# Performance work log

Hardware: AMD Instinct MI355X
Metric: run time of the kernel (lower is better)

## Reference

```python
import math
import jax, jax.numpy as jnp
import numpy as np

CT = {"SDD": 1000.0, "SCD": 500.0, "det_interval": 1.0, "num_det": 736}


def ramp_filter_np(ct, scale):
    # Standard equiangular fan-beam ramp filter (utility.ramp_filter):
    #   h[0] = 1/(8*db^2); h[n odd] = -1/(2*(pi*sin(n*db))^2); h[n even!=0] = 0
    db = ct["det_interval"] / ct["SDD"] * scale  # angular detector pitch at this scale
    n_det = int(ct["num_det"] // scale)
    n = np.arange(-(n_det - 1), n_det)  # length K = 2*n_det - 1
    h = np.zeros(n.shape, dtype=np.float32)
    h[n == 0] = 1.0 / (8.0 * db ** 2)
    odd = (n % 2) != 0
    h[odd] = -0.5 / (np.pi * np.sin(n[odd] * db)) ** 2
    return h


def setup_inputs() -> dict:
    key = jax.random.key(0)
    scale = 1
    batch, ch, view, det = 16, 1, 1152, CT["num_det"] // scale
    sinogram = jax.random.normal(key, (batch, ch, view, det), dtype=jnp.float32)
    delta_b = CT["det_interval"] / CT["SDD"]
    # recon_filter = ramp_filter * scale * delta_b, shaped [1,1,1,K] (OIHW)
    filt = ramp_filter_np(CT, scale) * scale * delta_b
    recon_filter = jnp.asarray(filt, dtype=jnp.float32)[None, None, None, :]
    return {"sinogram": sinogram, "recon_filter": recon_filter, "scale": scale}


def reference(sinogram, recon_filter, scale):
    det = sinogram.shape[-1]
    # cosine fan-beam pre-weighting
    s_range = (CT["det_interval"]
               * jnp.linspace((1.0 - det) / 2.0, (det - 1.0) / 2.0, det, dtype=jnp.float32)
               * scale) / CT["SDD"]
    cos_weight = (CT["SCD"] / 10000.0) * jnp.cos(s_range)  # [det]
    x = sinogram * cos_weight[None, None, None, :]
    # 1D ramp-filter convolution along detector axis (F.conv2d with 1xK kernel)
    K = recon_filter.shape[-1]
    pad = K // 2
    out = jax.lax.conv_general_dilated(
        x, recon_filter,
        window_strides=(1, 1),
        padding=[(0, 0), (pad, pad)],
        dimension_numbers=("NCHW", "OIHW", "NCHW"),
    )
    return out
```

## Files before the change

### kernel.cpp

```cpp
#include <hip/hip_runtime.h>

typedef unsigned short ushort_t;
typedef ushort_t u16x8 __attribute__((ext_vector_type(8)));
typedef __bf16 bf16x8 __attribute__((ext_vector_type(8)));
typedef float f32x4 __attribute__((ext_vector_type(4)));

#define DET 736
#define NPAD 768
#define NT 23
#define NRB 1152
#define CPB (NT * 64)


__global__ void prep_af(const float* __restrict__ sino, ushort_t* __restrict__ Af) {
    int c = blockIdx.x * blockDim.x + threadIdx.x;
    int rblk = c / CPB;
    int rem  = c - rblk * CPB;
    int t    = rem >> 6;
    int lane = rem & 63;
    int rr = lane & 15, quad = lane >> 4;
    const float* g = sino + (size_t)(rblk * 16 + rr) * DET + t * 32 + quad * 8;
    f32x4 lo = *(const f32x4*)g;
    f32x4 hi = *(const f32x4*)(g + 4);
    u16x8 v;
#pragma unroll
    for (int e = 0; e < 4; ++e) {
        v[e]     = __builtin_bit_cast(ushort_t, (__bf16)lo[e]);
        v[e + 4] = __builtin_bit_cast(ushort_t, (__bf16)hi[e]);
    }
    *(u16x8*)(Af + (size_t)c * 8) = v;
}

__global__ void prep_bf(const float* __restrict__ filt, ushort_t* __restrict__ Bf) {
    int c = blockIdx.x * blockDim.x + threadIdx.x;
    int cb  = c / CPB;
    int rem = c - cb * CPB;
    int t    = rem >> 6;
    int lane = rem & 63;
    int cc = lane & 15, quad = lane >> 4;
    int n = cb * 16 + cc;
    u16x8 v;
#pragma unroll
    for (int e = 0; e < 8; ++e) {
        int k = t * 32 + quad * 8 + e;
        float w = 0.05f * cosf(((float)k - 367.5f) * 0.001f);
        float val = (n < DET) ? filt[k - n + (DET - 1)] * w : 0.0f;
        v[e] = __builtin_bit_cast(ushort_t, (__bf16)val);
    }
    *(u16x8*)(Bf + (size_t)c * 8) = v;
}

__global__ __launch_bounds__(1024, 4) void gemm_frag(
    const ushort_t* __restrict__ Af,
    const ushort_t* __restrict__ Bf,
    float* __restrict__ C)
{
    __shared__ ushort_t Bs[4 * CPB * 8];

    const int tid  = threadIdx.x;
    const int lane = tid & 63;
    const int wid  = tid >> 6;
    const int quad = lane >> 4;
    const int l16  = lane & 15;

    const ushort_t* bsrc = Bf + (size_t)blockIdx.y * (4 * CPB * 8);
    for (int c = tid; c < 4 * CPB; c += 1024)
        *(u16x8*)(Bs + c * 8) = *(const u16x8*)(bsrc + (size_t)c * 8);
    __syncthreads();

    const int rblk0 = blockIdx.x * 64 + wid * 4;

    f32x4 acc[4][4];
#pragma unroll
    for (int i = 0; i < 4; ++i)
#pragma unroll
        for (int j = 0; j < 4; ++j)
            acc[i][j] = (f32x4){0.f, 0.f, 0.f, 0.f};

    const ushort_t* pA[4];
#pragma unroll
    for (int mi = 0; mi < 4; ++mi)
        pA[mi] = Af + ((size_t)(rblk0 + mi) * CPB + lane) * 8;
    const ushort_t* pB[4];
#pragma unroll
    for (int ni = 0; ni < 4; ++ni)
        pB[ni] = Bs + (ni * CPB + lane) * 8;

    for (int t = 0; t < NT; ++t) {
        u16x8 a[4], b[4];
#pragma unroll
        for (int mi = 0; mi < 4; ++mi)
            a[mi] = *(const u16x8*)(pA[mi] + t * 512);
#pragma unroll
        for (int ni = 0; ni < 4; ++ni)
            b[ni] = *(const u16x8*)(pB[ni] + t * 512);
#pragma unroll
        for (int mi = 0; mi < 4; ++mi)
#pragma unroll
            for (int ni = 0; ni < 4; ++ni)
                acc[mi][ni] = __builtin_amdgcn_mfma_f32_16x16x32_bf16(
                    __builtin_bit_cast(bf16x8, a[mi]),
                    __builtin_bit_cast(bf16x8, b[ni]),
                    acc[mi][ni], 0, 0, 0);
    }

    const int col0 = blockIdx.y * 64;
#pragma unroll
    for (int mi = 0; mi < 4; ++mi) {
#pragma unroll
        for (int ni = 0; ni < 4; ++ni) {
            int colg = col0 + ni * 16 + l16;
            if (colg < DET) {
#pragma unroll
                for (int r = 0; r < 4; ++r) {
                    size_t rowg = (size_t)(rblk0 + mi) * 16 + quad * 4 + r;
                    C[rowg * DET + colg] = acc[mi][ni][r];
                }
            }
        }
    }
}

extern "C" void kernel_launch(void* const* d_in, const int* in_sizes, int n_in,
                              void* d_out, int out_size, void* d_ws, size_t ws_size,
                              hipStream_t stream) {
    const float* sino = (const float*)d_in[0];
    const float* filt = (const float*)d_in[1];
    int total = in_sizes[0];
    int M = total / DET;

    ushort_t* Af = (ushort_t*)d_ws;
    ushort_t* Bf = Af + (size_t)NRB * CPB * 8;
    float* out = (float*)d_out;

    prep_af<<<(NRB * CPB) / 256, 256, 0, stream>>>(sino, Af);
    prep_bf<<<(48 * CPB) / 256, 256, 0, stream>>>(filt, Bf);

    dim3 grid(M / 1024, NPAD / 64);
    gemm_frag<<<grid, 1024, 0, stream>>>(Af, Bf, out);
}
```

Before: 138.6 us.

## Exploit ramp filter's zero even taps to split convolution into half-size parity GEMMs

The ramp filter is zero at every even nonzero offset, so each output only depends on inputs of opposite parity plus the center tap. The detector axis is split into even and odd halves, producing two half-K, half-N GEMMs (about a quarter of the MACs each), and the center tap is added in the epilogue from the original fp32 sinogram. The A fragments for the next k-step are also loaded ahead of time as a register prefetch. The cost is an extra sinogram read in the epilogue, strided stores to interleaved columns, and a more complex prep kernel.

After: 158.8 us. 1.15x slower.

```diff
diff --git a/kernel.cpp b/kernel.cpp
--- a/kernel.cpp
+++ b/kernel.cpp
@@ -6,69 +6,99 @@
 typedef float f32x4 __attribute__((ext_vector_type(4)));
 
 #define DET 736
-#define NPAD 768
-#define NT 23
+#define HALF 368
+#define HK 384
+#define NTT 12
+#define CPB2 (NTT * 64)
 #define NRB 1152
-#define CPB (NT * 64)
 
 
-__global__ void prep_af(const float* __restrict__ sino, ushort_t* __restrict__ Af) {
+__global__ void prep_af(const float* __restrict__ sino,
+                        ushort_t* __restrict__ Ae, ushort_t* __restrict__ Ao) {
     int c = blockIdx.x * blockDim.x + threadIdx.x;
-    int rblk = c / CPB;
-    int rem  = c - rblk * CPB;
-    int t    = rem >> 6;
-    int lane = rem & 63;
+    int rblk = c / CPB2;
+    int rem  = c - rblk * CPB2;
+    int t = rem >> 6, lane = rem & 63;
     int rr = lane & 15, quad = lane >> 4;
-    const float* g = sino + (size_t)(rblk * 16 + rr) * DET + t * 32 + quad * 8;
-    f32x4 lo = *(const f32x4*)g;
-    f32x4 hi = *(const f32x4*)(g + 4);
-    u16x8 v;
+    int j0 = t * 32 + quad * 8;
+    u16x8 ve, vo;
+    if (j0 < HALF) {
+        const float* g = sino + (size_t)(rblk * 16 + rr) * DET + 2 * j0;
+        float w[16];
+        *(f32x4*)(w)      = *(const f32x4*)(g);
+        *(f32x4*)(w + 4)  = *(const f32x4*)(g + 4);
+        *(f32x4*)(w + 8)  = *(const f32x4*)(g + 8);
+        *(f32x4*)(w + 12) = *(const f32x4*)(g + 12);
 #pragma unroll
-    for (int e = 0; e < 4; ++e) {
-        v[e]     = __builtin_bit_cast(ushort_t, (__bf16)lo[e]);
-        v[e + 4] = __builtin_bit_cast(ushort_t, (__bf16)hi[e]);
+        for (int e = 0; e < 8; ++e) {
+            vo[e] = __builtin_bit_cast(ushort_t, (__bf16)w[2 * e]);
+            ve[e] = __builtin_bit_cast(ushort_t, (__bf16)w[2 * e + 1]);
+        }
+    } else {
+#pragma unroll
+        for (int e = 0; e < 8; ++e) { ve[e] = 0; vo[e] = 0; }
     }
-    *(u16x8*)(Af + (size_t)c * 8) = v;
+    *(u16x8*)(Ae + (size_t)c * 8) = ve;
+    *(u16x8*)(Ao + (size_t)c * 8) = vo;
 }
 
-__global__ void prep_bf(const float* __restrict__ filt, ushort_t* __restrict__ Bf) {
+__global__ void prep_bf(const float* __restrict__ filt,
+                        ushort_t* __restrict__ Be, ushort_t* __restrict__ Bo) {
     int c = blockIdx.x * blockDim.x + threadIdx.x;
-    int cb  = c / CPB;
-    int rem = c - cb * CPB;
-    int t    = rem >> 6;
-    int lane = rem & 63;
-    int cc = lane & 15, quad = lane >> 4;
-    int n = cb * 16 + cc;
-    u16x8 v;
+    int cb  = c / CPB2;
+    int rem = c - cb * CPB2;
+    int t = rem >> 6, lane = rem & 63;
+    int i = cb * 16 + (lane & 15);
+    int quad = lane >> 4;
+    u16x8 ve, vo;
 #pragma unroll
     for (int e = 0; e < 8; ++e) {
-        int k = t * 32 + quad * 8 + e;
-        float w = 0.05f * cosf(((float)k - 367.5f) * 0.001f);
-        float val = (n < DET) ? filt[k - n + (DET - 1)] * w : 0.0f;
-        v[e] = __builtin_bit_cast(ushort_t, (__bf16)val);
+        int j = t * 32 + quad * 8 + e;
+        bool real = (j < HALF) && (i < HALF);
+        int de = 2 * (j - i) + 1 + 735;
+        int do_ = de - 2;
+        de  = de  < 0 ? 0 : (de  > 1470 ? 1470 : de);
+        do_ = do_ < 0 ? 0 : (do_ > 1470 ? 1470 : do_);
+        float ge = 0.05f * cosf(((float)(2 * j + 1) - 367.5f) * 0.001f);
+        float go = 0.05f * cosf(((float)(2 * j)     - 367.5f) * 0.001f);
+        float fe = filt[de] * ge;
+        float fo = filt[do_] * go;
+        ve[e] = real ? __builtin_bit_cast(ushort_t, (__bf16)fe) : (ushort_t)0;
+        vo[e] = real ? __builtin_bit_cast(ushort_t, (__bf16)fo) : (ushort_t)0;
     }
-    *(u16x8*)(Bf + (size_t)c * 8) = v;
+    *(u16x8*)(Be + (size_t)c * 8) = ve;
+    *(u16x8*)(Bo + (size_t)c * 8) = vo;
 }
 
-__global__ __launch_bounds__(1024, 4) void gemm_frag(
-    const ushort_t* __restrict__ Af,
-    const ushort_t* __restrict__ Bf,
+__global__ __launch_bounds__(1024, 4) void gemm_half(
+    const ushort_t* __restrict__ Ae, const ushort_t* __restrict__ Ao,
+    const ushort_t* __restrict__ Be, const ushort_t* __restrict__ Bo,
+    const float* __restrict__ sino, const float* __restrict__ filt,
     float* __restrict__ C)
 {
-    __shared__ ushort_t Bs[4 * CPB * 8];
+    __shared__ ushort_t Bs[8 * CPB2 * 8];
+
+    const int p    = blockIdx.z;
+    const ushort_t* Af = p ? Ao : Ae;
+    const ushort_t* Bf = p ? Bo : Be;
 
     const int tid  = threadIdx.x;
     const int lane = tid & 63;
     const int wid  = tid >> 6;
+    const int wm   = wid >> 1;
+    const int wn   = wid & 1;
     const int quad = lane >> 4;
     const int l16  = lane & 15;
 
-    const ushort_t* bsrc = Bf + (size_t)blockIdx.y * (4 * CPB * 8);
-    for (int c = tid; c < 4 * CPB; c += 1024)
-        *(u16x8*)(Bs + c * 8) = *(const u16x8*)(bsrc + (size_t)c * 8);
+    const int cbg0 = blockIdx.y * 8;
+    {
+        const ushort_t* bsrc = Bf + (size_t)cbg0 * CPB2 * 8;
+        for (int c = tid; c < 8 * CPB2; c += 1024)
+            *(u16x8*)(Bs + c * 8) = *(const u16x8*)(bsrc + (size_t)c * 8);
+    }
     __syncthreads();
 
-    const int rblk0 = blockIdx.x * 64 + wid * 4;
+    const int rblk0 = blockIdx.x * 32 + wm * 4;
 
     f32x4 acc[4][4];
 #pragma unroll
@@ -80,17 +110,25 @@
     const ushort_t* pA[4];
 #pragma unroll
     for (int mi = 0; mi < 4; ++mi)
-        pA[mi] = Af + ((size_t)(rblk0 + mi) * CPB + lane) * 8;
+        pA[mi] = Af + ((size_t)(rblk0 + mi) * CPB2 + lane) * 8;
     const ushort_t* pB[4];
 #pragma unroll
     for (int ni = 0; ni < 4; ++ni)
-        pB[ni] = Bs + (ni * CPB + lane) * 8;
+        pB[ni] = Bs + ((wn * 4 + ni) * CPB2 + lane) * 8;
 
-    for (int t = 0; t < NT; ++t) {
-        u16x8 a[4], b[4];
+    u16x8 acur[4];
 #pragma unroll
-        for (int mi = 0; mi < 4; ++mi)
-            a[mi] = *(const u16x8*)(pA[mi] + t * 512);
+    for (int mi = 0; mi < 4; ++mi)
+        acur[mi] = *(const u16x8*)(pA[mi]);
+
+    for (int t = 0; t < NTT; ++t) {
+        u16x8 anx[4];
+        if (t + 1 < NTT) {
+#pragma unroll
+            for (int mi = 0; mi < 4; ++mi)
+                anx[mi] = *(const u16x8*)(pA[mi] + (t + 1) * 512);
+        }
+        u16x8 b[4];
 #pragma unroll
         for (int ni = 0; ni < 4; ++ni)
             b[ni] = *(const u16x8*)(pB[ni] + t * 512);
@@ -99,22 +137,34 @@
 #pragma unroll
             for (int ni = 0; ni < 4; ++ni)
                 acc[mi][ni] = __builtin_amdgcn_mfma_f32_16x16x32_bf16(
-                    __builtin_bit_cast(bf16x8, a[mi]),
+                    __builtin_bit_cast(bf16x8, acur[mi]),
                     __builtin_bit_cast(bf16x8, b[ni]),
                     acc[mi][ni], 0, 0, 0);
+        if (t + 1 < NTT) {
+#pragma unroll
+            for (int mi = 0; mi < 4; ++mi) acur[mi] = anx[mi];
+        }
     }
 
-    const int col0 = blockIdx.y * 64;
+    const float h0 = filt[735];
+    float gwv[4];
+    int   ncol[4];
+#pragma unroll
+    for (int ni = 0; ni < 4; ++ni) {
+        int ic   = blockIdx.y * 128 + (wn * 4 + ni) * 16 + l16;
+        ncol[ni] = 2 * ic + p;
+        gwv[ni]  = h0 * 0.05f * cosf(((float)ncol[ni] - 367.5f) * 0.001f);
+    }
 #pragma unroll
     for (int mi = 0; mi < 4; ++mi) {
 #pragma unroll
         for (int ni = 0; ni < 4; ++ni) {
-            int colg = col0 + ni * 16 + l16;
-            if (colg < DET) {
+            if (ncol[ni] < DET) {
 #pragma unroll
                 for (int r = 0; r < 4; ++r) {
                     size_t rowg = (size_t)(rblk0 + mi) * 16 + quad * 4 + r;
-                    C[rowg * DET + colg] = acc[mi][ni][r];
+                    float xd = sino[rowg * DET + ncol[ni]];
+                    C[rowg * DET + ncol[ni]] = acc[mi][ni][r] + gwv[ni] * xd;
                 }
             }
         }
@@ -126,16 +176,20 @@
                               hipStream_t stream) {
     const float* sino = (const float*)d_in[0];
     const float* filt = (const float*)d_in[1];
-    int total = in_sizes[0];
-    int M = total / DET;
+    (void)in_sizes; (void)n_in; (void)out_size; (void)ws_size;
 
-    ushort_t* Af = (ushort_t*)d_ws;
-    ushort_t* Bf = Af + (size_t)NRB * CPB * 8;
+    const size_t ASZ = (size_t)NRB * CPB2 * 8;
+    const size_t BSZ = (size_t)24 * CPB2 * 8;
+
+    ushort_t* Ae = (ushort_t*)d_ws;
+    ushort_t* Ao = Ae + ASZ;
+    ushort_t* Be = Ao + ASZ;
+    ushort_t* Bo = Be + BSZ;
     float* out = (float*)d_out;
 
-    prep_af<<<(NRB * CPB) / 256, 256, 0, stream>>>(sino, Af);
-    prep_bf<<<(48 * CPB) / 256, 256, 0, stream>>>(filt, Bf);
+    prep_af<<<(NRB * CPB2) / 256, 256, 0, stream>>>(sino, Ae, Ao);
+    prep_bf<<<(24 * CPB2) / 256, 256, 0, stream>>>(filt, Be, Bo);
 
-    dim3 grid(M / 1024, NPAD / 64);
-    gemm_frag<<<grid, 1024, 0, stream>>>(Af, Bf, out);
+    dim3 grid(NRB / 32, 3, 2);
+    gemm_half<<<grid, 1024, 0, stream>>>(Ae, Ao, Be, Bo, sino, filt, out);
 }
```
